# Kernel tuning notes

Measured on AMD Instinct MI355X. Metric: run time of the kernel, lower is better.

## Reference

```python
import jax, jax.numpy as jnp
import numpy as np

D_MODEL = 2048
D_INNER = 2048
N_QK = 32
N_V = 32
D_STATE = 64
D_CONV = 4
CHUNK = 128
CONV_DIM = D_INNER + 2 * N_QK * D_STATE  # 6144
IN_OUT = 2 * D_INNER + 2 * N_QK * D_STATE + N_V  # 8224


def setup_inputs() -> dict:
    key = jax.random.key(0)
    ks = jax.random.split(key, 6)
    u = jax.random.normal(ks[0], (2, 4096, D_MODEL), dtype=jnp.float32)
    W_in = jax.random.normal(ks[1], (IN_OUT, D_MODEL), dtype=jnp.float32) * 0.02
    conv_w = jax.random.normal(ks[2], (CONV_DIM, D_CONV), dtype=jnp.float32) * 0.2
    conv_b = jax.random.normal(ks[3], (CONV_DIM,), dtype=jnp.float32) * 0.02
    D = jnp.ones((N_V,), dtype=jnp.float32)
    z_bias = jnp.zeros((D_INNER,), dtype=jnp.float32)
    W_out = jax.random.normal(ks[4], (D_MODEL, D_INNER), dtype=jnp.float32) * 0.02
    return {"u": u, "W_in": W_in, "conv_w": conv_w, "conv_b": conv_b,
            "D": D, "z_bias": z_bias, "W_out": W_out}


def causal_depthwise_conv(x, w, b):
    # x: [B, L, C]; w: [C, K]; b: [C]. Torch Conv1d(groups=C, padding=K-1)[..., :L]
    B, L, C = x.shape
    K = w.shape[1]
    xp = jnp.pad(x, ((0, 0), (K - 1, 0), (0, 0)))
    y = b[None, None, :]
    for k in range(K):
        y = y + xp[:, k:k + L, :] * w[None, None, :, k]
    return y


def ssd_chunk_scan(x, dt, B, C, chunk):
    # Mamba2 SSD with A = -1 per head.
    # x: [b,l,h,p], dt: [b,l,h] (positive), B,C: [b,l,h,n]
    b, l, h, p = x.shape
    n = B.shape[-1]
    nc = l // chunk
    x = x.reshape(b, nc, chunk, h, p)
    dt = dt.reshape(b, nc, chunk, h)
    B = B.reshape(b, nc, chunk, h, n)
    C = C.reshape(b, nc, chunk, h, n)
    a = -dt                                  # A * dt
    cum = jnp.cumsum(a, axis=2)              # [b,nc,q,h]
    xdt = x * dt[..., None]                  # dt_t * x_t
    # ---- intra-chunk (causal, decay exp(cum_q - cum_k), q >= k) ----
    CB = jnp.einsum('bcqhn,bckhn->bchqk', C, B)
    cumT = jnp.swapaxes(cum, 2, 3)           # [b,nc,h,q]
    diff = cumT[..., :, None] - cumT[..., None, :]   # [b,nc,h,q,k]
    mask = jnp.tril(jnp.ones((chunk, chunk), dtype=bool))
    decay = jnp.exp(jnp.where(mask, diff, -jnp.inf))
    y_intra = jnp.einsum('bchqk,bckhp->bcqhp', CB * decay, xdt)
    # ---- per-chunk final states ----
    state_decay = jnp.exp(cum[:, :, -1:, :] - cum)   # [b,nc,q,h]
    states = jnp.einsum('bckhn,bckhp->bchpn', B * state_decay[..., None], xdt)
    chunk_decay = jnp.exp(cum[:, :, -1, :])          # [b,nc,h]
    # ---- inter-chunk recurrence ----
    def step(carry, inp):
        st, cd = inp  # st [b,h,p,n], cd [b,h]
        new = carry * cd[:, :, None, None] + st
        return new, carry  # emit the state *entering* this chunk
    init = jnp.zeros((b, h, p, n), dtype=x.dtype)
    _, prev = jax.lax.scan(step, init,
                           (jnp.moveaxis(states, 1, 0), jnp.moveaxis(chunk_decay, 1, 0)))
    prev = jnp.moveaxis(prev, 0, 1)                  # [b,nc,h,p,n]
    y_inter = jnp.einsum('bcqhn,bchpn->bcqhp', C * jnp.exp(cum)[..., None], prev)
    return (y_intra + y_inter).reshape(b, l, h, p)


def reference(u, W_in, conv_w, conv_b, D, z_bias, W_out):
    b, l, _ = u.shape  # l divisible by CHUNK (padded_len == l)
    xBCzA = jnp.einsum('bld,od->blo', u, W_in)
    xBC = xBCzA[..., :CONV_DIM]
    z = xBCzA[..., CONV_DIM:CONV_DIM + D_INNER]
    A_log = xBCzA[..., CONV_DIM + D_INNER:]
    xBC = causal_depthwise_conv(xBC, conv_w, conv_b)  # activation = identity
    x = xBC[..., :D_INNER]
    Bm = xBC[..., D_INNER:D_INNER + N_QK * D_STATE]
    Cm = xBC[..., D_INNER + N_QK * D_STATE:]
    x = x.reshape(b, l, N_V, D_INNER // N_V)
    Bm = Bm.reshape(b, l, N_QK, D_STATE)
    Cm = Cm.reshape(b, l, N_QK, D_STATE)
    dt = jax.nn.softplus(A_log)                       # [b,l,h]
    x_scan = x / dt[..., None]
    y = ssd_chunk_scan(x_scan, dt, Bm, Cm, CHUNK)
    y = y + D[None, None, :, None] * x                # Du uses undivided x
    y = y.reshape(b, l, D_INNER)
    out = jnp.einsum('bli,oi->blo', y * jax.nn.silu(z + z_bias), W_out)
    return out
```

## Files before the change

### kernel.cpp

```cpp
#include <hip/hip_runtime.h>
#include <math.h>

#define D_MODEL  2048
#define D_INNER  2048
#define N_QK     32
#define N_V      32
#define D_STATE  64
#define D_CONV   4
#define CHUNK    128
#define CONV_DIM 6144
#define IN_OUT   8224
#define BATCH    2
#define SEQ      4096
#define M_ROWS   (BATCH*SEQ)
#define NCHUNK   (SEQ/CHUNK)

typedef unsigned short bf16_t;
typedef __attribute__((ext_vector_type(4))) float f32x4;
typedef __attribute__((ext_vector_type(8))) short bf16x8;

#define SWZ64(r,c)  ((((r)*64)  + (c)) ^ (((r)&7)<<3))
#define SWZ128(r,c) ((((r)*128) + (c)) ^ (((r)&7)<<3))

__device__ __forceinline__ float b2f(bf16_t u) {
    union { unsigned int i; float f; } w; w.i = ((unsigned int)u) << 16; return w.f;
}
__device__ __forceinline__ bf16_t f2b(float f) {
    unsigned int x = __float_as_uint(f);
    return (bf16_t)((x + 0x7FFFu + ((x >> 16) & 1u)) >> 16);
}
__device__ __forceinline__ void store4b(bf16_t* dst, float4 v) {
    ushort4 u; u.x = f2b(v.x); u.y = f2b(v.y); u.z = f2b(v.z); u.w = f2b(v.w);
    *reinterpret_cast<ushort4*>(dst) = u;
}

__device__ __forceinline__ void gload_lds16(const bf16_t* g, bf16_t* l) {
    __builtin_amdgcn_global_load_lds((const __attribute__((address_space(1))) void*)g,
                                     (__attribute__((address_space(3))) void*)l,
                                     16, 0, 0);
}

__global__ __launch_bounds__(256) void f2b3_kernel(const float* __restrict__ a0, bf16_t* __restrict__ o0, long n0,
                                                   const float* __restrict__ a1, bf16_t* __restrict__ o1, long n1,
                                                   const float* __restrict__ a2, bf16_t* __restrict__ o2, long n2)
{
    const long total = (n0 + n1 + n2) >> 2;
    for (long s = (long)blockIdx.x * 256 + threadIdx.x; s < total; s += (long)gridDim.x * 256) {
        long i = s << 2;
        const float* in; bf16_t* out;
        if (i < n0)           { in = a0 + i; out = o0 + i; }
        else if (i < n0 + n1) { i -= n0; in = a1 + i; out = o1 + i; }
        else                  { i -= n0 + n1; in = a2 + i; out = o2 + i; }
        float4 v = *reinterpret_cast<const float4*>(in);
        ushort4 o;
        o.x = f2b(v.x); o.y = f2b(v.y); o.z = f2b(v.z); o.w = f2b(v.w);
        *reinterpret_cast<ushort4*>(out) = o;
    }
}

template<int NTB, int K, bool OBF16>
__global__ __launch_bounds__(512, 2) void gemm256(const bf16_t* __restrict__ A,
                                                  const bf16_t* __restrict__ B,
                                                  void* __restrict__ Cv,
                                                  long ldc)
{
    constexpr int BK = 64;
    constexpr int NT = K / BK;
    __shared__ bf16_t As[2][2][8192];
    __shared__ bf16_t Bs[2][2][8192];

    const int nwg = gridDim.x;
    const int bid = blockIdx.x;
    const int wg  = ((nwg & 7) == 0) ? ((bid & 7) * (nwg >> 3) + (bid >> 3)) : bid;
    const int bm = (wg / NTB) * 256;
    const int bn = (wg % NTB) * 256;

    const int tid  = threadIdx.x;
    const int lane = tid & 63;
    const int wv   = tid >> 6;
    const int wr   = wv >> 2, wc = wv & 3;
    const int l15  = lane & 15, l4 = lane >> 4;

    f32x4 acc[8][4];
    #pragma unroll
    for (int i = 0; i < 8; ++i)
        #pragma unroll
        for (int j = 0; j < 4; ++j) acc[i][j] = (f32x4){0.f, 0.f, 0.f, 0.f};

    const bf16_t* Abase = A + (long)bm * K;
    const bf16_t* Bbase = B + (long)bn * K;

    auto stage_half = [&](int t, int buf, int kh) {
        #pragma unroll
        for (int it = 0; it < 2; ++it) {
            const int s   = it * 512 + tid;
            const int row = s >> 2;
            const int jp  = s & 3;
            const int jl  = jp ^ ((row >> 1) & 3);
            const long go = (long)row * K + t * BK + kh * 32 + jl * 8;
            gload_lds16(Abase + go, &As[buf][kh][s * 8]);
            gload_lds16(Bbase + go, &Bs[buf][kh][s * 8]);
        }
    };
    auto rdA = [&](int buf, int kh, int row) {
        const int jp = l4 ^ ((row >> 1) & 3);
        return *reinterpret_cast<const bf16x8*>(&As[buf][kh][(row * 4 + jp) * 8]);
    };
    auto rdB = [&](int buf, int kh, int row) {
        const int jp = l4 ^ ((row >> 1) & 3);
        return *reinterpret_cast<const bf16x8*>(&Bs[buf][kh][(row * 4 + jp) * 8]);
    };

    stage_half(0, 0, 0);
    stage_half(0, 0, 1);
    asm volatile("s_waitcnt vmcnt(4)" ::: "memory");
    __builtin_amdgcn_s_barrier();

    for (int t = 0; t < NT; ++t) {
        const int cur = t & 1;
        bf16x8 bfr[4], af[4];
        if (t + 1 < NT) stage_half(t + 1, cur ^ 1, 0);
        #pragma unroll
        for (int ni = 0; ni < 4; ++ni) bfr[ni] = rdB(cur, 0, wc * 64 + ni * 16 + l15);
        #pragma unroll
        for (int mi = 0; mi < 4; ++mi) af[mi] = rdA(cur, 0, wr * 128 + mi * 16 + l15);
        __builtin_amdgcn_s_setprio(1);
        #pragma unroll
        for (int mi = 0; mi < 4; ++mi)
            #pragma unroll
            for (int ni = 0; ni < 4; ++ni)
                acc[mi][ni] = __builtin_amdgcn_mfma_f32_16x16x32_bf16(
                    af[mi], bfr[ni], acc[mi][ni], 0, 0, 0);
        __builtin_amdgcn_s_setprio(0);
        #pragma unroll
        for (int mi = 0; mi < 4; ++mi) af[mi] = rdA(cur, 0, wr * 128 + 64 + mi * 16 + l15);
        __builtin_amdgcn_s_setprio(1);
        #pragma unroll
        for (int mi = 0; mi < 4; ++mi)
            #pragma unroll
            for (int ni = 0; ni < 4; ++ni)
                acc[4 + mi][ni] = __builtin_amdgcn_mfma_f32_16x16x32_bf16(
                    af[mi], bfr[ni], acc[4 + mi][ni], 0, 0, 0);
        __builtin_amdgcn_s_setprio(0);
        if (t + 1 < NT) {
            stage_half(t + 1, cur ^ 1, 1);
            asm volatile("s_waitcnt vmcnt(8)" ::: "memory");
        } else {
            asm volatile("s_waitcnt vmcnt(0)" ::: "memory");
        }
        __builtin_amdgcn_s_barrier();
        #pragma unroll
        for (int ni = 0; ni < 4; ++ni) bfr[ni] = rdB(cur, 1, wc * 64 + ni * 16 + l15);
        #pragma unroll
        for (int mi = 0; mi < 4; ++mi) af[mi] = rdA(cur, 1, wr * 128 + mi * 16 + l15);
        __builtin_amdgcn_s_setprio(1);
        #pragma unroll
        for (int mi = 0; mi < 4; ++mi)
            #pragma unroll
            for (int ni = 0; ni < 4; ++ni)
                acc[mi][ni] = __builtin_amdgcn_mfma_f32_16x16x32_bf16(
                    af[mi], bfr[ni], acc[mi][ni], 0, 0, 0);
        __builtin_amdgcn_s_setprio(0);
        #pragma unroll
        for (int mi = 0; mi < 4; ++mi) af[mi] = rdA(cur, 1, wr * 128 + 64 + mi * 16 + l15);
        __builtin_amdgcn_s_setprio(1);
        #pragma unroll
        for (int mi = 0; mi < 4; ++mi)
            #pragma unroll
            for (int ni = 0; ni < 4; ++ni)
                acc[4 + mi][ni] = __builtin_amdgcn_mfma_f32_16x16x32_bf16(
                    af[mi], bfr[ni], acc[4 + mi][ni], 0, 0, 0);
        __builtin_amdgcn_s_setprio(0);
        if (t + 1 < NT) { asm volatile("s_waitcnt vmcnt(4)" ::: "memory"); }
        __builtin_amdgcn_s_barrier();
    }

    #pragma unroll
    for (int mf = 0; mf < 8; ++mf) {
        const long grow0 = bm + wr * 128 + mf * 16 + l4 * 4;
        #pragma unroll
        for (int ni = 0; ni < 4; ++ni) {
            const int gcol = bn + wc * 64 + ni * 16 + l15;
            #pragma unroll
            for (int j = 0; j < 4; ++j) {
                if (OBF16)
                    ((bf16_t*)Cv)[(grow0 + j) * ldc + gcol] = f2b(acc[mf][ni][j]);
                else
                    ((float*)Cv)[(grow0 + j) * ldc + gcol] = acc[mf][ni][j];
            }
        }
    }
}

__global__ __launch_bounds__(256) void alog_partial(const bf16_t* __restrict__ A,
                                                    const bf16_t* __restrict__ Bt,
                                                    float* __restrict__ P)
{
    const int rb = blockIdx.x & 63, ks = blockIdx.x >> 6;
    const int bm = rb * 128;
    __shared__ bf16_t As[128 * 64];
    __shared__ bf16_t Bs[32 * 64];
    const int tid = threadIdx.x, lane = tid & 63, wv = tid >> 6;
    const int l15 = lane & 15, l4 = lane >> 4;

    f32x4 acc[2][2];
    #pragma unroll
    for (int mi = 0; mi < 2; ++mi)
        #pragma unroll
        for (int nj = 0; nj < 2; ++nj) acc[mi][nj] = (f32x4){0.f, 0.f, 0.f, 0.f};

    for (int it8 = 0; it8 < 8; ++it8) {
        const long kbase = (long)ks * 512 + it8 * 64;
        #pragma unroll
        for (int it = 0; it < 4; ++it) {
            const int s = it * 256 + tid;
            const int row = s >> 3, c16 = s & 7;
            gload_lds16(A + (long)(bm + row) * D_MODEL + kbase + (c16 ^ (row & 7)) * 8,
                        &As[s * 8]);
        }
        {
            const int row = tid >> 3, c16 = tid & 7;
            gload_lds16(Bt + (long)row * D_MODEL + kbase + (c16 ^ (row & 7)) * 8,
                        &Bs[tid * 8]);
        }
        __syncthreads();
        #pragma unroll
        for (int kk = 0; kk < 2; ++kk) {
            bf16x8 bf[2], af;
            #pragma unroll
            for (int nj = 0; nj < 2; ++nj) {
                const int row = nj * 16 + l15;
                bf[nj] = *reinterpret_cast<const bf16x8*>(&Bs[row * 64 + (((kk * 4 + l4) ^ (row & 7)) << 3)]);
            }
            #pragma unroll
            for (int mi = 0; mi < 2; ++mi) {
                const int row = wv * 32 + mi * 16 + l15;
                af = *reinterpret_cast<const bf16x8*>(&As[row * 64 + (((kk * 4 + l4) ^ (row & 7)) << 3)]);
                #pragma unroll
                for (int nj = 0; nj < 2; ++nj)
                    acc[mi][nj] = __builtin_amdgcn_mfma_f32_16x16x32_bf16(af, bf[nj], acc[mi][nj], 0, 0, 0);
            }
        }
        __syncthreads();
    }
    #pragma unroll
    for (int mi = 0; mi < 2; ++mi)
        #pragma unroll
        for (int nj = 0; nj < 2; ++nj)
            #pragma unroll
            for (int j = 0; j < 4; ++j) {
                const int row = bm + wv * 32 + mi * 16 + l4 * 4 + j;
                P[(long)ks * (M_ROWS * 32) + (long)row * 32 + nj * 16 + l15] = acc[mi][nj][j];
            }
}

__global__ __launch_bounds__(256) void alog_fin(const float* __restrict__ P,
                                                float* __restrict__ dt)
{
    const long i = (long)blockIdx.x * 256 + threadIdx.x;
    if (i < (long)M_ROWS * 32) {
        const long n = (long)M_ROWS * 32;
        const float a = P[i] + P[n + i] + P[2 * n + i] + P[3 * n + i];
        dt[i] = (a > 20.f) ? a : log1pf(expf(a));
    }
}

__device__ __forceinline__ float4 conv4v(const bf16_t* __restrict__ xb, long m, int l,
                                         int col, const float* __restrict__ cw,
                                         const float* __restrict__ cbv)
{
    float4 acc = *reinterpret_cast<const float4*>(cbv + col);
    float4 wc0 = *reinterpret_cast<const float4*>(cw + (long)col * 4);
    float4 wc1 = *reinterpret_cast<const float4*>(cw + (long)col * 4 + 4);
    float4 wc2 = *reinterpret_cast<const float4*>(cw + (long)col * 4 + 8);
    float4 wc3 = *reinterpret_cast<const float4*>(cw + (long)col * 4 + 12);
    const float t0[4] = {wc0.x, wc0.y, wc0.z, wc0.w};
    const float t1[4] = {wc1.x, wc1.y, wc1.z, wc1.w};
    const float t2[4] = {wc2.x, wc2.y, wc2.z, wc2.w};
    const float t3[4] = {wc3.x, wc3.y, wc3.z, wc3.w};
    #pragma unroll
    for (int tap = 0; tap < 4; ++tap) {
        if (l - 3 + tap < 0) continue;
        const bf16_t* p = xb + (m - 3 + tap) * (long)IN_OUT + col;
        ushort4 v = *reinterpret_cast<const ushort4*>(p);
        acc.x = fmaf(b2f(v.x), t0[tap], acc.x);
        acc.y = fmaf(b2f(v.y), t1[tap], acc.y);
        acc.z = fmaf(b2f(v.z), t2[tap], acc.z);
        acc.w = fmaf(b2f(v.w), t3[tap], acc.w);
    }
    return acc;
}

template<bool EXP>
__global__ __launch_bounds__(512, 4) void ssd_states(const bf16_t* __restrict__ xb,
                                                     const float* __restrict__ dtb,
                                                     const float* __restrict__ cw,
                                                     const float* __restrict__ cbv,
                                                     bf16_t* __restrict__ states,
                                                     float* __restrict__ cumbuf,
                                                     float* __restrict__ cdecay,
                                                     bf16_t* __restrict__ xtg,
                                                     bf16_t* __restrict__ bg)
{
    const int h = blockIdx.x, c = blockIdx.y, b = blockIdx.z;
    __shared__ bf16_t sx [128 * 64];
    __shared__ bf16_t sBr[128 * 64];
    __shared__ bf16_t sXT[64 * 128];
    __shared__ bf16_t sBT[64 * 128];
    __shared__ float  cum[CHUNK];
    __shared__ float  w0tot;
    const int t = threadIdx.x;
    const long mbase = (long)b * SEQ + (long)c * CHUNK;
    const long cb = ((long)b * NCHUNK + c) * N_QK + h;

    float v = 0.f;
    if (t < CHUNK) {
        v = -dtb[(mbase + t) * N_V + h];
        #pragma unroll
        for (int s = 1; s < 64; s <<= 1) {
            const float u2 = __shfl_up(v, s, 64);
            if ((t & 63) >= s) v += u2;
        }
        if (t == 63) w0tot = v;
    }
    for (int idx = t; idx < CHUNK * 16; idx += 512) {
        const int k = idx >> 4, q4 = (idx & 15) * 4;
        const long m = mbase + k;
        const int l = (int)(m & (SEQ - 1));
        float4 xv = conv4v(xb, m, l, h * 64 + q4, cw, cbv);
        float4 bv = conv4v(xb, m, l, D_INNER + h * 64 + q4, cw, cbv);
        store4b(&sx [SWZ64(k, q4)], xv);
        store4b(&sBr[SWZ64(k, q4)], bv);
    }
    __syncthreads();
    if (t >= 64 && t < CHUNK) v += w0tot;
    if (t < CHUNK) cum[t] = v;
    __syncthreads();
    const float clast = cum[CHUNK - 1];
    {
        const int j = t & 127;
        const int c8b = (t >> 7) * 2;
        const float ej = __expf(clast - cum[j]);
        #pragma unroll
        for (int it = 0; it < 2; ++it) {
            const int c8 = c8b + it;
            bf16x8 xv = *reinterpret_cast<const bf16x8*>(&sx [SWZ64(j, c8 * 8)]);
            bf16x8 bv = *reinterpret_cast<const bf16x8*>(&sBr[SWZ64(j, c8 * 8)]);
            #pragma unroll
            for (int e = 0; e < 8; ++e) {
                sXT[SWZ128(c8 * 8 + e, j)] = xv[e];
                sBT[SWZ128(c8 * 8 + e, j)] = f2b(b2f((bf16_t)bv[e]) * ej);
            }
        }
    }
    __syncthreads();

    const int lane = t & 63, wv = t >> 6;
    const int l15 = lane & 15, l4 = lane >> 4;
    const int prow  = (wv & 3) * 16;
    const int nbase = (wv >> 2) * 2;
    f32x4 acc[2];
    acc[0] = (f32x4){0.f, 0.f, 0.f, 0.f};
    acc[1] = (f32x4){0.f, 0.f, 0.f, 0.f};
    #pragma unroll
    for (int ks = 0; ks < 4; ++ks) {
        const int kc = ks * 32 + l4 * 8;
        bf16x8 af = *reinterpret_cast<const bf16x8*>(&sXT[SWZ128(prow + l15, kc)]);
        #pragma unroll
        for (int nj = 0; nj < 2; ++nj) {
            bf16x8 bf = *reinterpret_cast<const bf16x8*>(&sBT[SWZ128((nbase + nj) * 16 + l15, kc)]);
            acc[nj] = __builtin_amdgcn_mfma_f32_16x16x32_bf16(af, bf, acc[nj], 0, 0, 0);
        }
    }
    #pragma unroll
    for (int nj = 0; nj < 2; ++nj) {
        #pragma unroll
        for (int jj = 0; jj < 4; ++jj) {
            const int p = prow + l4 * 4 + jj;
            states[cb * 4096 + SWZ64(p, (nbase + nj) * 16 + l15)] = f2b(acc[nj][jj]);
        }
    }
    if constexpr (EXP) {
        #pragma unroll
        for (int it = 0; it < 2; ++it) {
            const int s = it * 512 + t;
            *reinterpret_cast<bf16x8*>(xtg + cb * 8192 + s * 8) =
                *reinterpret_cast<const bf16x8*>(&sXT[s * 8]);
            *reinterpret_cast<bf16x8*>(bg + cb * 8192 + s * 8) =
                *reinterpret_cast<const bf16x8*>(&sBr[s * 8]);
        }
    }
    if (t < CHUNK) cumbuf[cb * CHUNK + t] = cum[t];
    if (t == 0)   cdecay[cb] = __expf(clast);
}

__global__ __launch_bounds__(256) void ssd_scan(bf16_t* __restrict__ states,
                                                const float* __restrict__ cdecay)
{
    const int bid = blockIdx.x;
    const int bh = bid >> 3, q = bid & 7;
    const int b = bh >> 5, h = bh & 31;
    const int t = threadIdx.x;
    __shared__ bf16_t sst[NCHUNK * 512];
    __shared__ float  scd[NCHUNK];
    if (t < NCHUNK) scd[t] = cdecay[((long)b * NCHUNK + t) * N_QK + h];
    #pragma unroll
    for (int it = 0; it < 8; ++it) {
        const int slot = it * 256 + t;
        const int c = slot >> 6, off = (slot & 63) * 8;
        const long g = (((long)b * NCHUNK + c) * N_QK + h) * 4096 + q * 512 + off;
        gload_lds16(states + g, &sst[slot * 8]);
    }
    __syncthreads();
    float2 carry = make_float2(0.f, 0.f);
    for (int c = 0; c < NCHUNK; ++c) {
        ushort2* p = reinterpret_cast<ushort2*>(&sst[c * 512 + t * 2]);
        const ushort2 su = *p;
        ushort2 pv;
        pv.x = f2b(carry.x); pv.y = f2b(carry.y);
        *p = pv;
        const float cd = scd[c];
        carry.x = fmaf(carry.x, cd, b2f(su.x));
        carry.y = fmaf(carry.y, cd, b2f(su.y));
    }
    __syncthreads();
    #pragma unroll
    for (int it = 0; it < 8; ++it) {
        const int slot = it * 256 + t;
        const int c = slot >> 6, off = (slot & 63) * 8;
        const long g = (((long)b * NCHUNK + c) * N_QK + h) * 4096 + q * 512 + off;
        *reinterpret_cast<bf16x8*>(states + g) =
            *reinterpret_cast<const bf16x8*>(&sst[slot * 8]);
    }
}

template<bool EXP>
__global__ __launch_bounds__(512, 4) void ssd_out(const bf16_t* __restrict__ xb,
                                                  const float* __restrict__ cumbuf,
                                                  const bf16_t* __restrict__ prevst,
                                                  const float* __restrict__ Dvec,
                                                  const float* __restrict__ zbias,
                                                  const float* __restrict__ cw,
                                                  const float* __restrict__ cbv,
                                                  const bf16_t* __restrict__ xtg,
                                                  const bf16_t* __restrict__ bg,
                                                  bf16_t* __restrict__ yz)
{
    const int h = blockIdx.x, c = blockIdx.y, b = blockIdx.z;
    __shared__ bf16_t sC[128 * 64];
    __shared__ bf16_t sB[128 * 64];
    __shared__ bf16_t sXQ[128 * 64];
    __shared__ bf16_t sXT[64 * 128];
    __shared__ bf16_t sP[64 * 64];
    __shared__ float  cum[CHUNK];
    const int t = threadIdx.x;
    const long mbase = (long)b * SEQ + (long)c * CHUNK;
    const long cb = ((long)b * NCHUNK + c) * N_QK + h;
    if (t < CHUNK) cum[t] = cumbuf[cb * CHUNK + t];
    gload_lds16(prevst + cb * 4096 + t * 8, &sP[t * 8]);
    if constexpr (EXP) {
        #pragma unroll
        for (int it = 0; it < 2; ++it) {
            const int s = it * 512 + t;
            gload_lds16(bg  + cb * 8192 + s * 8, &sB [s * 8]);
            gload_lds16(xtg + cb * 8192 + s * 8, &sXT[s * 8]);
        }
        for (int idx = t; idx < CHUNK * 16; idx += 512) {
            const int k = idx >> 4, q4 = (idx & 15) * 4;
            const long m = mbase + k;
            const int l = (int)(m & (SEQ - 1));
            float4 cv = conv4v(xb, m, l, 2 * D_INNER + h * 64 + q4, cw, cbv);
            store4b(&sC[SWZ64(k, q4)], cv);
        }
        __syncthreads();
    } else {
        for (int idx = t; idx < CHUNK * 16; idx += 512) {
            const int k = idx >> 4, q4 = (idx & 15) * 4;
            const long m = mbase + k;
            const int l = (int)(m & (SEQ - 1));
            float4 xv = conv4v(xb, m, l, h * 64 + q4, cw, cbv);
            float4 bv = conv4v(xb, m, l, D_INNER + h * 64 + q4, cw, cbv);
            float4 cv = conv4v(xb, m, l, 2 * D_INNER + h * 64 + q4, cw, cbv);
            store4b(&sXQ[SWZ64(k, q4)], xv);
            store4b(&sB [SWZ64(k, q4)], bv);
            store4b(&sC [SWZ64(k, q4)], cv);
        }
        __syncthreads();
        {
            const int j = t & 127;
            const int c8b = (t >> 7) * 2;
            #pragma unroll
            for (int it = 0; it < 2; ++it) {
                const int c8 = c8b + it;
                bf16x8 v = *reinterpret_cast<const bf16x8*>(&sXQ[SWZ64(j, c8 * 8)]);
                #pragma unroll
                for (int e = 0; e < 8; ++e) sXT[SWZ128(c8 * 8 + e, j)] = v[e];
            }
        }
        __syncthreads();
    }

    const int lane = t & 63, wv = t >> 6;
    const int w16 = wv * 16, l15 = lane & 15, l4 = lane >> 4;
    bf16_t* sQ = sXQ;

    f32x4 yac[4], iac[4];
    #pragma unroll
    for (int np = 0; np < 4; ++np) {
        yac[np] = (f32x4){0.f, 0.f, 0.f, 0.f};
        iac[np] = (f32x4){0.f, 0.f, 0.f, 0.f};
    }

    #pragma unroll
    for (int H = 0; H < 2; ++H) {
        if (H == 1 && wv < 4) break;
        const int j0 = H * 64;
        f32x4 sac[4];
        #pragma unroll
        for (int nj = 0; nj < 4; ++nj) sac[nj] = (f32x4){0.f, 0.f, 0.f, 0.f};
        #pragma unroll
        for (int kk = 0; kk < 2; ++kk) {
            const int kc = kk * 32 + l4 * 8;
            bf16x8 af0 = *reinterpret_cast<const bf16x8*>(&sC[SWZ64(w16 + l15, kc)]);
            #pragma unroll
            for (int nj = 0; nj < 4; ++nj) {
                if (j0 + nj * 16 <= w16 + 15) {
                    bf16x8 bfj = *reinterpret_cast<const bf16x8*>(&sB[SWZ64(j0 + nj * 16 + l15, kc)]);
                    sac[nj] = __builtin_amdgcn_mfma_f32_16x16x32_bf16(af0, bfj, sac[nj], 0, 0, 0);
                }
            }
        }
        #pragma unroll
        for (int nj = 0; nj < 4; ++nj) {
            const int jcol = nj * 16 + l15;
            const int jg = j0 + jcol;
            #pragma unroll
            for (int jj = 0; jj < 4; ++jj) {
                const int i = w16 + l4 * 4 + jj;
                const float q = (jg <= i) ? __expf(cum[i] - cum[jg]) * sac[nj][jj] : 0.f;
                sQ[SWZ64(i, jcol)] = f2b(q);
            }
        }
        #pragma unroll
        for (int kk = 0; kk < 2; ++kk) {
            const int kc = kk * 32 + l4 * 8;
            bf16x8 qa = *reinterpret_cast<const bf16x8*>(&sQ[SWZ64(w16 + l15, kc)]);
            #pragma unroll
            for (int np = 0; np < 4; ++np) {
                bf16x8 xf = *reinterpret_cast<const bf16x8*>(&sXT[SWZ128(np * 16 + l15, j0 + kc)]);
                yac[np] = __builtin_amdgcn_mfma_f32_16x16x32_bf16(qa, xf, yac[np], 0, 0, 0);
            }
        }
    }
    #pragma unroll
    for (int kk = 0; kk < 2; ++kk) {
        const int kc = kk * 32 + l4 * 8;
        bf16x8 cf = *reinterpret_cast<const bf16x8*>(&sC[SWZ64(w16 + l15, kc)]);
        #pragma unroll
        for (int np = 0; np < 4; ++np) {
            bf16x8 pf = *reinterpret_cast<const bf16x8*>(&sP[SWZ64(np * 16 + l15, kc)]);
            iac[np] = __builtin_amdgcn_mfma_f32_16x16x32_bf16(cf, pf, iac[np], 0, 0, 0);
        }
    }
    const float dh = Dvec[h];
    #pragma unroll
    for (int jj = 0; jj < 4; ++jj) {
        const int i = w16 + l4 * 4 + jj;
        const float ei = __expf(cum[i]);
        const long m = mbase + i;
        const bf16_t* zr = xb + m * (long)IN_OUT + CONV_DIM + h * 64;
        bf16_t* orow = yz + m * (long)D_INNER + h * 64;
        #pragma unroll
        for (int np = 0; np < 4; ++np) {
            const int p = np * 16 + l15;
            const float xval = b2f(sXT[SWZ128(p, i)]);
            const float y = yac[np][jj] + ei * iac[np][jj] + dh * xval;
            const float zv = b2f(zr[p]) + zbias[h * 64 + p];
            const float s = zv / (1.f + __expf(-zv));
            orow[p] = f2b(y * s);
        }
    }
}

extern "C" void kernel_launch(void* const* d_in, const int* in_sizes, int n_in,
                              void* d_out, int out_size, void* d_ws, size_t ws_size,
                              hipStream_t stream)
{
    const float* u      = (const float*)d_in[0];
    const float* W_in   = (const float*)d_in[1];
    const float* conv_w = (const float*)d_in[2];
    const float* conv_b = (const float*)d_in[3];
    const float* Dv     = (const float*)d_in[4];
    const float* z_bias = (const float*)d_in[5];
    const float* W_out  = (const float*)d_in[6];
    float* out = (float*)d_out;

    char* w = (char*)d_ws;
    bf16_t* xbcza = (bf16_t*)w;  w += (long)M_ROWS * IN_OUT * 2;
    bf16_t* wob   = (bf16_t*)w;  w += (long)2048 * 2048 * 2;
    char* ureg = w;  w += 67239936;
    bf16_t* ub  = (bf16_t*)ureg;
    bf16_t* wib = (bf16_t*)(ureg + (long)M_ROWS * D_MODEL * 2);
    bf16_t* yzb = (bf16_t*)ureg;
    float*  cumb   = (float*)(ureg + (long)M_ROWS * D_INNER * 2);
    bf16_t* states = (bf16_t*)(cumb + (long)BATCH * NCHUNK * N_QK * CHUNK);
    float*  cdec   = (float*)(states + (long)BATCH * NCHUNK * N_QK * 4096);
    float* partials = (float*)(ureg + 50331648);
    float* dtb      = (float*)(ureg + 54525952);
    const long base_bytes = (long)(w - (char*)d_ws);
    const long exp_bytes  = 2L * 2048 * 8192 * 2;
    const bool use_exp = ((long)ws_size >= base_bytes + exp_bytes);
    bf16_t* xtg = (bf16_t*)w;
    bf16_t* bg  = xtg + (long)2048 * 8192;

    {
        const long n0 = (long)M_ROWS * D_MODEL;
        const long n1 = (long)IN_OUT * D_MODEL;
        const long n2 = (long)D_MODEL * D_INNER;
        f2b3_kernel<<<2048, 256, 0, stream>>>(u, ub, n0, W_in, wib, n1, W_out, wob, n2);
    }

    gemm256<32, D_MODEL, true><<<(M_ROWS / 256) * 32, 512, 0, stream>>>(
        ub, wib, xbcza, IN_OUT);

    alog_partial<<<256, 256, 0, stream>>>(ub, wib + (long)8192 * D_MODEL, partials);
    alog_fin<<<(M_ROWS * 32 + 255) / 256, 256, 0, stream>>>(partials, dtb);

    if (use_exp) {
        ssd_states<true><<<dim3(N_QK, NCHUNK, BATCH), 512, 0, stream>>>(
            xbcza, dtb, conv_w, conv_b, states, cumb, cdec, xtg, bg);
        ssd_scan<<<BATCH * N_QK * 8, 256, 0, stream>>>(states, cdec);
        ssd_out<true><<<dim3(N_QK, NCHUNK, BATCH), 512, 0, stream>>>(
            xbcza, cumb, states, Dv, z_bias, conv_w, conv_b, xtg, bg, yzb);
    } else {
        ssd_states<false><<<dim3(N_QK, NCHUNK, BATCH), 512, 0, stream>>>(
            xbcza, dtb, conv_w, conv_b, states, cumb, cdec, nullptr, nullptr);
        ssd_scan<<<BATCH * N_QK * 8, 256, 0, stream>>>(states, cdec);
        ssd_out<false><<<dim3(N_QK, NCHUNK, BATCH), 512, 0, stream>>>(
            xbcza, cumb, states, Dv, z_bias, conv_w, conv_b, nullptr, nullptr, yzb);
    }

    gemm256<8, D_INNER, false><<<(M_ROWS / 256) * 8, 512, 0, stream>>>(
        yzb, wob, out, D_MODEL);
}
```

Measured before the change: 713.1 us.

## Fuse softplus finalize into ssd_states and reuse shared buffers for transposes

Removes the alog_fin kernel by summing the split-K partials and applying softplus directly inside ssd_states, avoiding a launch and a dt round trip through global memory. The transposed x and B tiles now overwrite the original shared buffers via register staging, halving shared memory so more blocks can be resident (launch bounds raised to 6). The global export of B and transposed x is moved earlier. This adds an extra barrier and recomputes softplus per head block.

```diff
diff --git a/kernel.cpp b/kernel.cpp
--- a/kernel.cpp
+++ b/kernel.cpp
@@ -254,17 +254,6 @@
             }
 }
 
-__global__ __launch_bounds__(256) void alog_fin(const float* __restrict__ P,
-                                                float* __restrict__ dt)
-{
-    const long i = (long)blockIdx.x * 256 + threadIdx.x;
-    if (i < (long)M_ROWS * 32) {
-        const long n = (long)M_ROWS * 32;
-        const float a = P[i] + P[n + i] + P[2 * n + i] + P[3 * n + i];
-        dt[i] = (a > 20.f) ? a : log1pf(expf(a));
-    }
-}
-
 __device__ __forceinline__ float4 conv4v(const bf16_t* __restrict__ xb, long m, int l,
                                          int col, const float* __restrict__ cw,
                                          const float* __restrict__ cbv)
@@ -292,8 +281,8 @@
 }
 
 template<bool EXP>
-__global__ __launch_bounds__(512, 4) void ssd_states(const bf16_t* __restrict__ xb,
-                                                     const float* __restrict__ dtb,
+__global__ __launch_bounds__(512, 6) void ssd_states(const bf16_t* __restrict__ xb,
+                                                     const float* __restrict__ P,
                                                      const float* __restrict__ cw,
                                                      const float* __restrict__ cbv,
                                                      bf16_t* __restrict__ states,
@@ -305,8 +294,6 @@
     const int h = blockIdx.x, c = blockIdx.y, b = blockIdx.z;
     __shared__ bf16_t sx [128 * 64];
     __shared__ bf16_t sBr[128 * 64];
-    __shared__ bf16_t sXT[64 * 128];
-    __shared__ bf16_t sBT[64 * 128];
     __shared__ float  cum[CHUNK];
     __shared__ float  w0tot;
     const int t = threadIdx.x;
@@ -315,7 +302,10 @@
 
     float v = 0.f;
     if (t < CHUNK) {
-        v = -dtb[(mbase + t) * N_V + h];
+        const long n = (long)M_ROWS * 32;
+        const long pi = (mbase + t) * N_V + h;
+        const float a = P[pi] + P[n + pi] + P[2 * n + pi] + P[3 * n + pi];
+        v = -((a > 20.f) ? a : log1pf(expf(a)));
         #pragma unroll
         for (int s = 1; s < 64; s <<= 1) {
             const float u2 = __shfl_up(v, s, 64);
@@ -335,25 +325,44 @@
     __syncthreads();
     if (t >= 64 && t < CHUNK) v += w0tot;
     if (t < CHUNK) cum[t] = v;
+    const int j = t & 127;
+    const int c8b = (t >> 7) * 2;
+    bf16x8 rx[2], rb[2];
+    #pragma unroll
+    for (int it = 0; it < 2; ++it) {
+        rx[it] = *reinterpret_cast<const bf16x8*>(&sx [SWZ64(j, (c8b + it) * 8)]);
+        rb[it] = *reinterpret_cast<const bf16x8*>(&sBr[SWZ64(j, (c8b + it) * 8)]);
+    }
+    if constexpr (EXP) {
+        #pragma unroll
+        for (int it = 0; it < 2; ++it) {
+            const int s = it * 512 + t;
+            *reinterpret_cast<bf16x8*>(bg + cb * 8192 + s * 8) =
+                *reinterpret_cast<const bf16x8*>(&sBr[s * 8]);
+        }
+    }
     __syncthreads();
     const float clast = cum[CHUNK - 1];
-    {
-        const int j = t & 127;
-        const int c8b = (t >> 7) * 2;
-        const float ej = __expf(clast - cum[j]);
+    const float ej = __expf(clast - cum[j]);
+    #pragma unroll
+    for (int it = 0; it < 2; ++it) {
+        const int c8 = c8b + it;
+        #pragma unroll
+        for (int e = 0; e < 8; ++e) {
+            sx [SWZ128(c8 * 8 + e, j)] = rx[it][e];
+            sBr[SWZ128(c8 * 8 + e, j)] = f2b(b2f((bf16_t)rb[it][e]) * ej);
+        }
+    }
+    __syncthreads();
+
+    if constexpr (EXP) {
         #pragma unroll
         for (int it = 0; it < 2; ++it) {
-            const int c8 = c8b + it;
-            bf16x8 xv = *reinterpret_cast<const bf16x8*>(&sx [SWZ64(j, c8 * 8)]);
-            bf16x8 bv = *reinterpret_cast<const bf16x8*>(&sBr[SWZ64(j, c8 * 8)]);
-            #pragma unroll
-            for (int e = 0; e < 8; ++e) {
-                sXT[SWZ128(c8 * 8 + e, j)] = xv[e];
-                sBT[SWZ128(c8 * 8 + e, j)] = f2b(b2f((bf16_t)bv[e]) * ej);
-            }
-        }
-    }
-    __syncthreads();
+            const int s = it * 512 + t;
+            *reinterpret_cast<bf16x8*>(xtg + cb * 8192 + s * 8) =
+                *reinterpret_cast<const bf16x8*>(&sx[s * 8]);
+        }
+    }
 
     const int lane = t & 63, wv = t >> 6;
     const int l15 = lane & 15, l4 = lane >> 4;
@@ -365,10 +374,10 @@
     #pragma unroll
     for (int ks = 0; ks < 4; ++ks) {
         const int kc = ks * 32 + l4 * 8;
-        bf16x8 af = *reinterpret_cast<const bf16x8*>(&sXT[SWZ128(prow + l15, kc)]);
+        bf16x8 af = *reinterpret_cast<const bf16x8*>(&sx[SWZ128(prow + l15, kc)]);
         #pragma unroll
         for (int nj = 0; nj < 2; ++nj) {
-            bf16x8 bf = *reinterpret_cast<const bf16x8*>(&sBT[SWZ128((nbase + nj) * 16 + l15, kc)]);
+            bf16x8 bf = *reinterpret_cast<const bf16x8*>(&sBr[SWZ128((nbase + nj) * 16 + l15, kc)]);
             acc[nj] = __builtin_amdgcn_mfma_f32_16x16x32_bf16(af, bf, acc[nj], 0, 0, 0);
         }
     }
@@ -378,16 +387,6 @@
         for (int jj = 0; jj < 4; ++jj) {
             const int p = prow + l4 * 4 + jj;
             states[cb * 4096 + SWZ64(p, (nbase + nj) * 16 + l15)] = f2b(acc[nj][jj]);
-        }
-    }
-    if constexpr (EXP) {
-        #pragma unroll
-        for (int it = 0; it < 2; ++it) {
-            const int s = it * 512 + t;
-            *reinterpret_cast<bf16x8*>(xtg + cb * 8192 + s * 8) =
-                *reinterpret_cast<const bf16x8*>(&sXT[s * 8]);
-            *reinterpret_cast<bf16x8*>(bg + cb * 8192 + s * 8) =
-                *reinterpret_cast<const bf16x8*>(&sBr[s * 8]);
         }
     }
     if (t < CHUNK) cumbuf[cb * CHUNK + t] = cum[t];
@@ -605,8 +604,7 @@
     float*  cumb   = (float*)(ureg + (long)M_ROWS * D_INNER * 2);
     bf16_t* states = (bf16_t*)(cumb + (long)BATCH * NCHUNK * N_QK * CHUNK);
     float*  cdec   = (float*)(states + (long)BATCH * NCHUNK * N_QK * 4096);
-    float* partials = (float*)(ureg + 50331648);
-    float* dtb      = (float*)(ureg + 54525952);
+    float* partials = (float*)(ureg + 58720256);
     const long base_bytes = (long)(w - (char*)d_ws);
     const long exp_bytes  = 2L * 2048 * 8192 * 2;
     const bool use_exp = ((long)ws_size >= base_bytes + exp_bytes);
@@ -624,17 +622,16 @@
         ub, wib, xbcza, IN_OUT);
 
     alog_partial<<<256, 256, 0, stream>>>(ub, wib + (long)8192 * D_MODEL, partials);
-    alog_fin<<<(M_ROWS * 32 + 255) / 256, 256, 0, stream>>>(partials, dtb);
 
     if (use_exp) {
         ssd_states<true><<<dim3(N_QK, NCHUNK, BATCH), 512, 0, stream>>>(
-            xbcza, dtb, conv_w, conv_b, states, cumb, cdec, xtg, bg);
+            xbcza, partials, conv_w, conv_b, states, cumb, cdec, xtg, bg);
         ssd_scan<<<BATCH * N_QK * 8, 256, 0, stream>>>(states, cdec);
         ssd_out<true><<<dim3(N_QK, NCHUNK, BATCH), 512, 0, stream>>>(
             xbcza, cumb, states, Dv, z_bias, conv_w, conv_b, xtg, bg, yzb);
     } else {
         ssd_states<false><<<dim3(N_QK, NCHUNK, BATCH), 512, 0, stream>>>(
-            xbcza, dtb, conv_w, conv_b, states, cumb, cdec, nullptr, nullptr);
+            xbcza, partials, conv_w, conv_b, states, cumb, cdec, nullptr, nullptr);
         ssd_scan<<<BATCH * N_QK * 8, 256, 0, stream>>>(states, cdec);
         ssd_out<false><<<dim3(N_QK, NCHUNK, BATCH), 512, 0, stream>>>(
             xbcza, cumb, states, Dv, z_bias, conv_w, conv_b, nullptr, nullptr, yzb);
```

Result: no change. 709.2 us (-0.5%).
